# Optimization experiments

Hardware: AMD Instinct MI355X
Metric: run time of the kernel (lower is better)

The kernel has to match this reference:

```python
import jax, jax.numpy as jnp
import numpy as np

B, D, F, T, H = 256, 128, 8, 128, 128


def setup_inputs() -> dict:
    key = jax.random.key(0)
    ks = jax.random.split(key, 6)
    inp = jax.random.normal(ks[0], (B, D, F, T), jnp.float32)
    # encode_attn: Linear(F*T + 2*H -> 1); weight laid out as [hidden | cell | x]
    w_attn = jax.random.normal(ks[1], (F * T + 2 * H,), jnp.float32) * 0.02
    b_attn = jax.random.normal(ks[2], (), jnp.float32) * 0.02
    # LSTM (single layer), PyTorch gate order i, f, g, o
    W_ih = jax.random.normal(ks[3], (4 * H, D * F), jnp.float32) * 0.02
    W_hh = jax.random.normal(ks[4], (4 * H, H), jnp.float32) * 0.02
    b_ih = jax.random.normal(ks[5], (4 * H,), jnp.float32) * 0.02
    b_hh = jnp.zeros((4 * H,), jnp.float32)
    return {"input": inp, "w_attn": w_attn, "b_attn": b_attn,
            "W_ih": W_ih, "W_hh": W_hh, "b_ih": b_ih, "b_hh": b_hh}


def reference(input, w_attn, b_attn, W_ih, W_hh, b_ih, b_hh):
    Bd, Dd, Fd, Td = input.shape
    Hd = W_hh.shape[1]
    # split attention weight per cat order: (hidden_state, cell_state, x)
    w_h = w_attn[:Hd]
    w_c = w_attn[Hd:2 * Hd]
    w_x = w_attn[2 * Hd:]
    x_flat = input.reshape(Bd, Dd, Fd * Td)           # [B, D, F*T]
    ex = x_flat @ w_x                                  # [B, D], constant over t
    xs = jnp.moveaxis(input, 3, 0)                     # [T, B, D, F]

    def step(carry, x_t):
        h, c = carry                                   # [B, H] each
        # attention logits: h/c contributions are per-batch scalars broadcast over drives
        e = ex + (h @ w_h + c @ w_c + b_attn)[:, None]  # [B, D]
        a = jax.nn.softmax(e, axis=-1)                 # softmax over drives
        x_hat = (a[:, :, None] * x_t).reshape(Bd, Dd * Fd)  # [B, D*F]
        gates = x_hat @ W_ih.T + h @ W_hh.T + b_ih + b_hh   # [B, 4H]
        i, f, g, o = jnp.split(gates, 4, axis=-1)
        c_new = jax.nn.sigmoid(f) * c + jax.nn.sigmoid(i) * jnp.tanh(g)
        h_new = jax.nn.sigmoid(o) * jnp.tanh(c_new)
        return (h_new, c_new), h_new

    h0 = jnp.zeros((Bd, Hd), input.dtype)
    c0 = jnp.zeros((Bd, Hd), input.dtype)
    _, hs = jax.lax.scan(step, (h0, c0), xs)           # hs: [T, B, H]
    return jnp.transpose(hs, (1, 0, 2))                # [B, T, H] == hidden_states[:, 1:]
```

## Files before the change

### kernel.cpp

```cpp
#include <hip/hip_runtime.h>
#include <cstdint>
#include <cstddef>

#define Bn 256
#define Dn 128
#define Fn 8
#define Tn 128
#define Hn 128
#define Kn 1024
#define Mn 512
#define GXP 130

typedef float f32x4 __attribute__((ext_vector_type(4)));
typedef short s16x8 __attribute__((ext_vector_type(8)));
typedef _Float16 h16x2 __attribute__((ext_vector_type(2)));

#if defined(__has_builtin)
#if __has_builtin(__builtin_amdgcn_fdot2)
#define HAVE_FDOT2 1
#else
#define HAVE_FDOT2 0
#endif
#else
#define HAVE_FDOT2 0
#endif

__device__ __forceinline__ unsigned short f32_to_bf16_rne(float f) {
  union { float f; uint32_t u; } v; v.f = f;
  uint32_t u = v.u;
  u += 0x7fffu + ((u >> 16) & 1u);
  return (unsigned short)(u >> 16);
}
__device__ __forceinline__ float bf16_to_f32(unsigned short h) {
  union { uint32_t u; float f; } v; v.u = ((uint32_t)h) << 16;
  return v.f;
}
__device__ __forceinline__ float sigm(float x) { return 1.0f / (1.0f + __expf(-x)); }
__device__ __forceinline__ float tanh_fast(float x) { return 1.0f - 2.0f / (__expf(2.0f * x) + 1.0f); }

__global__ __launch_bounds__(256) void k_softmax_a(const float* __restrict__ input,
                                                   const float* __restrict__ w_attn,
                                                   float* __restrict__ a_out) {
  __shared__ float wx[Kn];
  __shared__ float exs[Dn];
  __shared__ float red[8];
  const int tid = threadIdx.x;
  const int b = blockIdx.x;
  ((float4*)wx)[tid] = ((const float4*)(w_attn + 2 * Hn))[tid];
  __syncthreads();
  const int w = tid >> 6, lane = tid & 63;
  const float4* wx4 = (const float4*)wx;
  for (int it = 0; it < 32; ++it) {
    const int d = it * 4 + w;
    const float4* xp = (const float4*)(input + ((size_t)b * Dn + d) * Kn);
    float acc = 0.f;
#pragma unroll
    for (int r = 0; r < 4; ++r) {
      float4 x = xp[lane + r * 64];
      float4 ww = wx4[lane + r * 64];
      acc += x.x * ww.x + x.y * ww.y + x.z * ww.z + x.w * ww.w;
    }
#pragma unroll
    for (int off = 32; off; off >>= 1) acc += __shfl_xor(acc, off);
    if (lane == 0) exs[d] = acc;
  }
  __syncthreads();
  float v = (tid < Dn) ? exs[tid] : -3.4e38f;
  float m = v;
#pragma unroll
  for (int off = 32; off; off >>= 1) m = fmaxf(m, __shfl_xor(m, off));
  if (lane == 0) red[w] = m;
  __syncthreads();
  m = fmaxf(fmaxf(red[0], red[1]), fmaxf(red[2], red[3]));
  float e = (tid < Dn) ? __expf(v - m) : 0.f;
  float s = e;
#pragma unroll
  for (int off = 32; off; off >>= 1) s += __shfl_xor(s, off);
  if (lane == 0) red[4 + w] = s;
  __syncthreads();
  s = red[4] + red[5] + red[6] + red[7];
  if (tid < Dn) a_out[b * Dn + tid] = e / s;
}

__global__ __launch_bounds__(256) void k_prep_wih(const float* __restrict__ W_ih,
                                                  unsigned short* __restrict__ whi,
                                                  unsigned short* __restrict__ wlo) {
  const int gid = blockIdx.x * 256 + threadIdx.x;
  const int lane = gid & 63;
  const int kt = (gid >> 6) & 31;
  const int mt = gid >> 11;
  const int row = mt * 16 + (lane & 15);
  const int col = kt * 32 + (lane >> 4) * 8;
  const float* src = W_ih + row * Kn + col;
  unsigned short hi8[8], lo8[8];
#pragma unroll
  for (int j = 0; j < 8; ++j) {
    float wv = src[j];
    unsigned short h = f32_to_bf16_rne(wv);
    hi8[j] = h;
    lo8[j] = f32_to_bf16_rne(wv - bf16_to_f32(h));
  }
  uint4 ph, pl;
  ph.x = (uint32_t)hi8[0] | ((uint32_t)hi8[1] << 16);
  ph.y = (uint32_t)hi8[2] | ((uint32_t)hi8[3] << 16);
  ph.z = (uint32_t)hi8[4] | ((uint32_t)hi8[5] << 16);
  ph.w = (uint32_t)hi8[6] | ((uint32_t)hi8[7] << 16);
  pl.x = (uint32_t)lo8[0] | ((uint32_t)lo8[1] << 16);
  pl.y = (uint32_t)lo8[2] | ((uint32_t)lo8[3] << 16);
  pl.z = (uint32_t)lo8[4] | ((uint32_t)lo8[5] << 16);
  pl.w = (uint32_t)lo8[6] | ((uint32_t)lo8[7] << 16);
  ((uint4*)whi)[gid] = ph;
  ((uint4*)wlo)[gid] = pl;
}

#define SM_A    133120
#define SM_G    133632
#define SM_H2   135680
#define SM_H32  135936
#define SM_TOT  136512

__global__ __launch_bounds__(512, 2) void k_fused(
    const float* __restrict__ input, const float* __restrict__ a_in,
    const unsigned short* __restrict__ whi, const unsigned short* __restrict__ wlo,
    const float* __restrict__ W_hh, const float* __restrict__ b_ih,
    const float* __restrict__ b_hh, float* __restrict__ out) {
  __shared__ __align__(16) unsigned char smem[SM_TOT];
  _Float16* gx = (_Float16*)smem;
  unsigned short* bb = (unsigned short*)smem;
  float* a_lds = (float*)(smem + SM_A);
  float* gstep = (float*)(smem + SM_G);
  _Float16* h2l = (_Float16*)(smem + SM_H2);
  float* h32 = (float*)(smem + SM_H32);

  const int tid = threadIdx.x;
  const int b = blockIdx.x;
  const int w = tid >> 6;
  const int lane = tid & 63;
  const int quad = lane >> 4;
  const int l15 = lane & 15;

  if (tid < Dn) a_lds[tid] = a_in[b * Dn + tid];

  f32x4 acc[4][8];
#pragma unroll
  for (int i = 0; i < 4; ++i)
#pragma unroll
    for (int j = 0; j < 8; ++j) {
      f32x4 z = {0.f, 0.f, 0.f, 0.f};
      acc[i][j] = z;
    }

  const int st_t = ((tid >> 6) & 1) * 64 + (tid & 63);
  const int kb2 = tid >> 7;
  const float* xb = input + (size_t)b * Kn * Tn;

  __syncthreads();

  for (int kt = 0; kt < 16; ++kt) {
    const int k0 = kt * 64;
#pragma unroll
    for (int hf = 0; hf < 2; ++hf) {
      const int kb = kb2 + hf * 4;
      const float av = a_lds[kt * 8 + kb];
      const float* col = xb + (size_t)(k0 + kb * 8) * Tn + st_t;
      unsigned short hx[8];
#pragma unroll
      for (int jj = 0; jj < 8; ++jj) hx[jj] = f32_to_bf16_rne(av * col[jj * Tn]);
      uint4 pk;
      pk.x = (uint32_t)hx[0] | ((uint32_t)hx[1] << 16);
      pk.y = (uint32_t)hx[2] | ((uint32_t)hx[3] << 16);
      pk.z = (uint32_t)hx[4] | ((uint32_t)hx[5] << 16);
      pk.w = (uint32_t)hx[6] | ((uint32_t)hx[7] << 16);
      ((uint4*)bb)[kb * 128 + st_t] = pk;
    }
    __syncthreads();
#pragma unroll
    for (int kf = 0; kf < 2; ++kf) {
      const int ktg = kt * 2 + kf;
      s16x8 afh[4], afl[4];
#pragma unroll
      for (int mt = 0; mt < 4; ++mt) {
        const int mtg = w * 4 + mt;
        const size_t fo = ((size_t)(mtg * 32 + ktg) * 64 + lane) * 8;
        afh[mt] = *(const s16x8*)(whi + fo);
        afl[mt] = *(const s16x8*)(wlo + fo);
      }
      s16x8 bfr[8];
#pragma unroll
      for (int nt = 0; nt < 8; ++nt) {
        const int chunk = (kf * 4 + quad) * 128 + nt * 16 + l15;
        bfr[nt] = *(const s16x8*)(bb + chunk * 8);
      }
#pragma unroll
      for (int mt = 0; mt < 4; ++mt)
#pragma unroll
        for (int nt = 0; nt < 8; ++nt) {
          acc[mt][nt] = __builtin_amdgcn_mfma_f32_16x16x32_bf16(afh[mt], bfr[nt], acc[mt][nt], 0, 0, 0);
          acc[mt][nt] = __builtin_amdgcn_mfma_f32_16x16x32_bf16(afl[mt], bfr[nt], acc[mt][nt], 0, 0, 0);
        }
    }
    __syncthreads();
  }

#pragma unroll
  for (int mt = 0; mt < 4; ++mt)
#pragma unroll
    for (int nt = 0; nt < 8; ++nt)
#pragma unroll
      for (int r = 0; r < 4; ++r) {
        const int j = w * 64 + mt * 16 + quad * 4 + r;
        const int t = nt * 16 + l15;
        gx[j * GXP + t] = (_Float16)acc[mt][nt][r];
      }

  const int j = tid;
  const float bsum = b_ih[j] + b_hh[j];
#if HAVE_FDOT2
  h16x2 wreg[64];
  {
    const float2* wrow = (const float2*)(W_hh + (size_t)j * Hn);
#pragma unroll
    for (int kk = 0; kk < 64; ++kk) {
      float2 w2 = wrow[kk];
      h16x2 t2;
      t2.x = (_Float16)w2.x;
      t2.y = (_Float16)w2.y;
      wreg[kk] = t2;
    }
  }
#else
  float wreg[128];
  {
    const float4* wrow = (const float4*)(W_hh + (size_t)j * Hn);
#pragma unroll
    for (int kk = 0; kk < 32; ++kk) {
      float4 w4 = wrow[kk];
      wreg[kk * 4 + 0] = w4.x;
      wreg[kk * 4 + 1] = w4.y;
      wreg[kk * 4 + 2] = w4.z;
      wreg[kk * 4 + 3] = w4.w;
    }
  }
#endif
  if (tid < Dn) {
    h2l[tid] = (_Float16)0.f;
    h32[tid] = 0.f;
  }
  float c_st = 0.f;
  __syncthreads();

  float* outp = out + (size_t)b * Tn * Hn;
  for (int t = 0; t < Tn; ++t) {
    float a0 = bsum + (float)gx[j * GXP + t];
    float a1 = 0.f, a2 = 0.f, a3 = 0.f;
#if HAVE_FDOT2
    const h16x2* hc = (const h16x2*)h2l;
#pragma unroll
    for (int kk = 0; kk < 16; ++kk) {
      a0 = __builtin_amdgcn_fdot2(wreg[kk * 4 + 0], hc[kk * 4 + 0], a0, false);
      a1 = __builtin_amdgcn_fdot2(wreg[kk * 4 + 1], hc[kk * 4 + 1], a1, false);
      a2 = __builtin_amdgcn_fdot2(wreg[kk * 4 + 2], hc[kk * 4 + 2], a2, false);
      a3 = __builtin_amdgcn_fdot2(wreg[kk * 4 + 3], hc[kk * 4 + 3], a3, false);
    }
#else
    const float4* hc4 = (const float4*)h32;
#pragma unroll
    for (int kk = 0; kk < 32; ++kk) {
      float4 h4 = hc4[kk];
      a0 = fmaf(wreg[kk * 4 + 0], h4.x, a0);
      a1 = fmaf(wreg[kk * 4 + 1], h4.y, a1);
      a2 = fmaf(wreg[kk * 4 + 2], h4.z, a2);
      a3 = fmaf(wreg[kk * 4 + 3], h4.w, a3);
    }
#endif
    gstep[j] = a0 + a1 + a2 + a3;
    __syncthreads();
    if (tid < Hn) {
      const int d = tid;
      const float gi = gstep[d];
      const float gf = gstep[Hn + d];
      const float gg = gstep[2 * Hn + d];
      const float go = gstep[3 * Hn + d];
      c_st = sigm(gf) * c_st + sigm(gi) * tanh_fast(gg);
      const float hnew = sigm(go) * tanh_fast(c_st);
      outp[t * Hn + d] = hnew;
      h2l[d] = (_Float16)hnew;
      h32[d] = hnew;
    }
    __syncthreads();
  }
}

extern "C" void kernel_launch(void* const* d_in, const int* in_sizes, int n_in,
                              void* d_out, int out_size, void* d_ws, size_t ws_size,
                              hipStream_t stream) {
  (void)in_sizes; (void)n_in; (void)out_size; (void)ws_size;
  const float* input = (const float*)d_in[0];
  const float* w_attn = (const float*)d_in[1];
  const float* W_ih = (const float*)d_in[3];
  const float* W_hh = (const float*)d_in[4];
  const float* b_ih = (const float*)d_in[5];
  const float* b_hh = (const float*)d_in[6];
  float* out = (float*)d_out;

  float* a_ws = (float*)d_ws;
  unsigned short* whi = (unsigned short*)((char*)d_ws + 131072);
  unsigned short* wlo = (unsigned short*)((char*)d_ws + 131072 + 1048576);

  k_softmax_a<<<Bn, 256, 0, stream>>>(input, w_attn, a_ws);
  k_prep_wih<<<256, 256, 0, stream>>>(W_ih, whi, wlo);
  k_fused<<<Bn, 512, 0, stream>>>(input, a_ws, whi, wlo, W_hh, b_ih, b_hh, out);
}
```

Measured before the change: 398.9 us.

## Split fused kernel into parallel gate GEMM and separate recurrence kernel

Splits the single per-batch fused kernel (input-projection GEMM plus LSTM recurrence) into a gate kernel launched with four blocks per batch that each own a quarter of the gate rows, and a separate recurrence kernel that reads the fp16 gate projections through global memory. The gate kernel double-buffers the LDS tile so the next k-slice is loaded while the current one feeds the MFMAs, and it XOR-swizzles LDS addresses to reduce bank conflicts. The attention-logit dot products now run one wave per (batch, drive) row across many more blocks, with the softmax moved into the gate kernel. W_hh is pre-packed to fp16 in a transposed layout for coalesced loads. The cost is an extra global round trip for the gate projections and more kernel launches, in exchange for more parallelism in the GEMM phase.

```diff
diff --git a/kernel.cpp b/kernel.cpp
--- a/kernel.cpp
+++ b/kernel.cpp
@@ -9,7 +9,6 @@
 #define Hn 128
 #define Kn 1024
 #define Mn 512
-#define GXP 130
 
 typedef float f32x4 __attribute__((ext_vector_type(4)));
 typedef short s16x8 __attribute__((ext_vector_type(8)));
@@ -31,55 +30,30 @@
   u += 0x7fffu + ((u >> 16) & 1u);
   return (unsigned short)(u >> 16);
 }
-__device__ __forceinline__ float bf16_to_f32(unsigned short h) {
-  union { uint32_t u; float f; } v; v.u = ((uint32_t)h) << 16;
-  return v.f;
-}
 __device__ __forceinline__ float sigm(float x) { return 1.0f / (1.0f + __expf(-x)); }
 __device__ __forceinline__ float tanh_fast(float x) { return 1.0f - 2.0f / (__expf(2.0f * x) + 1.0f); }
 
-__global__ __launch_bounds__(256) void k_softmax_a(const float* __restrict__ input,
-                                                   const float* __restrict__ w_attn,
-                                                   float* __restrict__ a_out) {
+__global__ __launch_bounds__(256) void k_ex(const float* __restrict__ input,
+                                            const float* __restrict__ w_attn,
+                                            float* __restrict__ ex) {
   __shared__ float wx[Kn];
-  __shared__ float exs[Dn];
-  __shared__ float red[8];
   const int tid = threadIdx.x;
-  const int b = blockIdx.x;
   ((float4*)wx)[tid] = ((const float4*)(w_attn + 2 * Hn))[tid];
   __syncthreads();
   const int w = tid >> 6, lane = tid & 63;
+  const int gid = blockIdx.x * 4 + w;
+  const float4* xp = (const float4*)(input + (size_t)gid * Kn);
   const float4* wx4 = (const float4*)wx;
-  for (int it = 0; it < 32; ++it) {
-    const int d = it * 4 + w;
-    const float4* xp = (const float4*)(input + ((size_t)b * Dn + d) * Kn);
-    float acc = 0.f;
-#pragma unroll
-    for (int r = 0; r < 4; ++r) {
-      float4 x = xp[lane + r * 64];
-      float4 ww = wx4[lane + r * 64];
-      acc += x.x * ww.x + x.y * ww.y + x.z * ww.z + x.w * ww.w;
-    }
-#pragma unroll
-    for (int off = 32; off; off >>= 1) acc += __shfl_xor(acc, off);
-    if (lane == 0) exs[d] = acc;
-  }
-  __syncthreads();
-  float v = (tid < Dn) ? exs[tid] : -3.4e38f;
-  float m = v;
-#pragma unroll
-  for (int off = 32; off; off >>= 1) m = fmaxf(m, __shfl_xor(m, off));
-  if (lane == 0) red[w] = m;
-  __syncthreads();
-  m = fmaxf(fmaxf(red[0], red[1]), fmaxf(red[2], red[3]));
-  float e = (tid < Dn) ? __expf(v - m) : 0.f;
-  float s = e;
-#pragma unroll
-  for (int off = 32; off; off >>= 1) s += __shfl_xor(s, off);
-  if (lane == 0) red[4 + w] = s;
-  __syncthreads();
-  s = red[4] + red[5] + red[6] + red[7];
-  if (tid < Dn) a_out[b * Dn + tid] = e / s;
+  float acc = 0.f;
+#pragma unroll
+  for (int r = 0; r < 4; ++r) {
+    float4 x = xp[lane + r * 64];
+    float4 ww = wx4[lane + r * 64];
+    acc += x.x * ww.x + x.y * ww.y + x.z * ww.z + x.w * ww.w;
+  }
+#pragma unroll
+  for (int off = 32; off; off >>= 1) acc += __shfl_xor(acc, off);
+  if (lane == 0) ex[gid] = acc;
 }
 
 __global__ __launch_bounds__(256) void k_prep_wih(const float* __restrict__ W_ih,
@@ -98,7 +72,8 @@
     float wv = src[j];
     unsigned short h = f32_to_bf16_rne(wv);
     hi8[j] = h;
-    lo8[j] = f32_to_bf16_rne(wv - bf16_to_f32(h));
+    union { uint32_t u; float f; } hb; hb.u = ((uint32_t)h) << 16;
+    lo8[j] = f32_to_bf16_rne(wv - hb.f);
   }
   uint4 ph, pl;
   ph.x = (uint32_t)hi8[0] | ((uint32_t)hi8[1] << 16);
@@ -113,146 +88,212 @@
   ((uint4*)wlo)[gid] = pl;
 }
 
-#define SM_A    133120
-#define SM_G    133632
-#define SM_H2   135680
-#define SM_H32  135936
-#define SM_TOT  136512
-
-__global__ __launch_bounds__(512, 2) void k_fused(
-    const float* __restrict__ input, const float* __restrict__ a_in,
+__global__ __launch_bounds__(256) void k_prep_whh(const float* __restrict__ W_hh,
+                                                  uint32_t* __restrict__ whhp) {
+  const int g = blockIdx.x * 256 + threadIdx.x;
+  const int j = g & 511, kk = g >> 9;
+  float2 wv = ((const float2*)(W_hh + (size_t)j * Hn))[kk];
+  h16x2 t2; t2.x = (_Float16)wv.x; t2.y = (_Float16)wv.y;
+  union { h16x2 h; uint32_t u; } cv; cv.h = t2;
+  whhp[kk * 512 + j] = cv.u;
+}
+
+__global__ __launch_bounds__(256, 3) void k_gates(
+    const float* __restrict__ input, const float* __restrict__ ex,
     const unsigned short* __restrict__ whi, const unsigned short* __restrict__ wlo,
-    const float* __restrict__ W_hh, const float* __restrict__ b_ih,
-    const float* __restrict__ b_hh, float* __restrict__ out) {
-  __shared__ __align__(16) unsigned char smem[SM_TOT];
-  _Float16* gx = (_Float16*)smem;
-  unsigned short* bb = (unsigned short*)smem;
-  float* a_lds = (float*)(smem + SM_A);
-  float* gstep = (float*)(smem + SM_G);
-  _Float16* h2l = (_Float16*)(smem + SM_H2);
-  float* h32 = (float*)(smem + SM_H32);
+    unsigned short* __restrict__ gx) {
+  __shared__ __align__(16) unsigned char smem[34816];
+  __shared__ float a_lds[Dn];
+  __shared__ float sred[8];
+  unsigned short* buf0 = (unsigned short*)smem;
+  unsigned short* buf1 = buf0 + 8192;
+  _Float16* lds_out = (_Float16*)smem;
 
   const int tid = threadIdx.x;
-  const int b = blockIdx.x;
+  const int b = blockIdx.x >> 2;
+  const int p = blockIdx.x & 3;
   const int w = tid >> 6;
   const int lane = tid & 63;
   const int quad = lane >> 4;
   const int l15 = lane & 15;
 
-  if (tid < Dn) a_lds[tid] = a_in[b * Dn + tid];
-
-  f32x4 acc[4][8];
-#pragma unroll
-  for (int i = 0; i < 4; ++i)
-#pragma unroll
-    for (int j = 0; j < 8; ++j) {
-      f32x4 z = {0.f, 0.f, 0.f, 0.f};
-      acc[i][j] = z;
-    }
-
-  const int st_t = ((tid >> 6) & 1) * 64 + (tid & 63);
-  const int kb2 = tid >> 7;
+  float v = (tid < Dn) ? ex[b * Dn + tid] : -3.4e38f;
+  float m = v;
+#pragma unroll
+  for (int off = 32; off; off >>= 1) m = fmaxf(m, __shfl_xor(m, off));
+  if (lane == 0) sred[w] = m;
+  __syncthreads();
+  m = fmaxf(fmaxf(sred[0], sred[1]), fmaxf(sred[2], sred[3]));
+  float e = (tid < Dn) ? __expf(v - m) : 0.f;
+  float s = e;
+#pragma unroll
+  for (int off = 32; off; off >>= 1) s += __shfl_xor(s, off);
+  if (lane == 0) sred[4 + w] = s;
+  __syncthreads();
+  s = sred[4] + sred[5] + sred[6] + sred[7];
+  if (tid < Dn) a_lds[tid] = e / s;
+
+  f32x4 acc[2][8];
+#pragma unroll
+  for (int i = 0; i < 2; ++i)
+#pragma unroll
+    for (int j = 0; j < 8; ++j) { f32x4 z = {0.f, 0.f, 0.f, 0.f}; acc[i][j] = z; }
+
+  const int kb = tid >> 5;
+  const int t0 = (tid & 31) * 4;
   const float* xb = input + (size_t)b * Kn * Tn;
 
   __syncthreads();
 
-  for (int kt = 0; kt < 16; ++kt) {
-    const int k0 = kt * 64;
-#pragma unroll
-    for (int hf = 0; hf < 2; ++hf) {
-      const int kb = kb2 + hf * 4;
-      const float av = a_lds[kt * 8 + kb];
-      const float* col = xb + (size_t)(k0 + kb * 8) * Tn + st_t;
+  {
+    float4 xr[8];
+    const float* src = xb + (size_t)(kb * 8) * Tn + t0;
+#pragma unroll
+    for (int j = 0; j < 8; ++j) xr[j] = *(const float4*)(src + (size_t)j * Tn);
+    const float av = a_lds[kb];
+#pragma unroll
+    for (int i = 0; i < 4; ++i) {
       unsigned short hx[8];
 #pragma unroll
-      for (int jj = 0; jj < 8; ++jj) hx[jj] = f32_to_bf16_rne(av * col[jj * Tn]);
+      for (int j = 0; j < 8; ++j) hx[j] = f32_to_bf16_rne(av * ((const float*)&xr[j])[i]);
       uint4 pk;
       pk.x = (uint32_t)hx[0] | ((uint32_t)hx[1] << 16);
       pk.y = (uint32_t)hx[2] | ((uint32_t)hx[3] << 16);
       pk.z = (uint32_t)hx[4] | ((uint32_t)hx[5] << 16);
       pk.w = (uint32_t)hx[6] | ((uint32_t)hx[7] << 16);
-      ((uint4*)bb)[kb * 128 + st_t] = pk;
-    }
-    __syncthreads();
+      const int tsw = (t0 + i) ^ ((kb & 1) << 2);
+      *(uint4*)(buf0 + (size_t)(kb * 128 + tsw) * 8) = pk;
+    }
+  }
+  __syncthreads();
+
+  for (int kt = 0; kt < 16; ++kt) {
+    unsigned short* cur = (kt & 1) ? buf1 : buf0;
+    unsigned short* nxt = (kt & 1) ? buf0 : buf1;
+    float4 xr[8];
+    if (kt < 15) {
+      const float* src = xb + (size_t)((kt + 1) * 64 + kb * 8) * Tn + t0;
+#pragma unroll
+      for (int j = 0; j < 8; ++j) xr[j] = *(const float4*)(src + (size_t)j * Tn);
+    }
 #pragma unroll
     for (int kf = 0; kf < 2; ++kf) {
       const int ktg = kt * 2 + kf;
-      s16x8 afh[4], afl[4];
-#pragma unroll
-      for (int mt = 0; mt < 4; ++mt) {
-        const int mtg = w * 4 + mt;
+      s16x8 afh[2], afl[2];
+#pragma unroll
+      for (int mt = 0; mt < 2; ++mt) {
+        const int mtg = p * 8 + w * 2 + mt;
         const size_t fo = ((size_t)(mtg * 32 + ktg) * 64 + lane) * 8;
         afh[mt] = *(const s16x8*)(whi + fo);
         afl[mt] = *(const s16x8*)(wlo + fo);
       }
       s16x8 bfr[8];
+      const int kbr = kf * 4 + quad;
 #pragma unroll
       for (int nt = 0; nt < 8; ++nt) {
-        const int chunk = (kf * 4 + quad) * 128 + nt * 16 + l15;
-        bfr[nt] = *(const s16x8*)(bb + chunk * 8);
-      }
-#pragma unroll
-      for (int mt = 0; mt < 4; ++mt)
+        const int tsw = (nt * 16 + l15) ^ ((kbr & 1) << 2);
+        bfr[nt] = *(const s16x8*)(cur + (size_t)(kbr * 128 + tsw) * 8);
+      }
+#pragma unroll
+      for (int mt = 0; mt < 2; ++mt)
 #pragma unroll
         for (int nt = 0; nt < 8; ++nt) {
           acc[mt][nt] = __builtin_amdgcn_mfma_f32_16x16x32_bf16(afh[mt], bfr[nt], acc[mt][nt], 0, 0, 0);
           acc[mt][nt] = __builtin_amdgcn_mfma_f32_16x16x32_bf16(afl[mt], bfr[nt], acc[mt][nt], 0, 0, 0);
         }
     }
+    if (kt < 15) {
+      const float av = a_lds[(kt + 1) * 8 + kb];
+#pragma unroll
+      for (int i = 0; i < 4; ++i) {
+        unsigned short hx[8];
+#pragma unroll
+        for (int j = 0; j < 8; ++j) hx[j] = f32_to_bf16_rne(av * ((const float*)&xr[j])[i]);
+        uint4 pk;
+        pk.x = (uint32_t)hx[0] | ((uint32_t)hx[1] << 16);
+        pk.y = (uint32_t)hx[2] | ((uint32_t)hx[3] << 16);
+        pk.z = (uint32_t)hx[4] | ((uint32_t)hx[5] << 16);
+        pk.w = (uint32_t)hx[6] | ((uint32_t)hx[7] << 16);
+        const int tsw = (t0 + i) ^ ((kb & 1) << 2);
+        *(uint4*)(nxt + (size_t)(kb * 128 + tsw) * 8) = pk;
+      }
+    }
     __syncthreads();
   }
 
 #pragma unroll
-  for (int mt = 0; mt < 4; ++mt)
+  for (int mt = 0; mt < 2; ++mt)
 #pragma unroll
     for (int nt = 0; nt < 8; ++nt)
 #pragma unroll
       for (int r = 0; r < 4; ++r) {
-        const int j = w * 64 + mt * 16 + quad * 4 + r;
-        const int t = nt * 16 + l15;
-        gx[j * GXP + t] = (_Float16)acc[mt][nt][r];
-      }
-
+        const int jl = (w * 2 + mt) * 16 + quad * 4 + r;
+        lds_out[jl * 136 + nt * 16 + l15] = (_Float16)acc[mt][nt][r];
+      }
+  __syncthreads();
+  {
+    const int jr = tid >> 1, half = tid & 1;
+    const uint4* lsrc = (const uint4*)(lds_out + jr * 136 + half * 64);
+    uint4* gdst = (uint4*)(gx + ((size_t)(b * Mn + p * 128 + jr)) * Tn + half * 64);
+#pragma unroll
+    for (int i = 0; i < 8; ++i) gdst[i] = lsrc[i];
+  }
+}
+
+__global__ __launch_bounds__(512) void k_rec(
+    const unsigned short* __restrict__ gx, const uint32_t* __restrict__ whhp,
+    const float* __restrict__ b_ih, const float* __restrict__ b_hh,
+    float* __restrict__ out) {
+  __shared__ __align__(16) unsigned short gxl[512 * 132];
+  __shared__ float gstep[Mn];
+  __shared__ __align__(4) _Float16 h2l[Hn];
+  __shared__ float h32[Hn];
+
+  const int tid = threadIdx.x;
+  const int b = blockIdx.x;
+
+  {
+    const int seg = tid & 3, rr = tid >> 2;
+#pragma unroll
+    for (int it = 0; it < 4; ++it) {
+      const int row = it * 128 + rr;
+      const uint4* gsrc = (const uint4*)(gx + ((size_t)b * Mn + row) * Tn + seg * 32);
+      uint2* dst = (uint2*)(gxl + row * 132 + seg * 32);
+#pragma unroll
+      for (int q = 0; q < 4; ++q) {
+        uint4 v = gsrc[q];
+        uint2 a0 = {v.x, v.y}, a1 = {v.z, v.w};
+        dst[q * 2] = a0;
+        dst[q * 2 + 1] = a1;
+      }
+    }
+  }
   const int j = tid;
   const float bsum = b_ih[j] + b_hh[j];
 #if HAVE_FDOT2
   h16x2 wreg[64];
-  {
-    const float2* wrow = (const float2*)(W_hh + (size_t)j * Hn);
-#pragma unroll
-    for (int kk = 0; kk < 64; ++kk) {
-      float2 w2 = wrow[kk];
-      h16x2 t2;
-      t2.x = (_Float16)w2.x;
-      t2.y = (_Float16)w2.y;
-      wreg[kk] = t2;
-    }
+#pragma unroll
+  for (int kk = 0; kk < 64; ++kk) {
+    union { uint32_t u; h16x2 h; } cv; cv.u = whhp[kk * 512 + j];
+    wreg[kk] = cv.h;
   }
 #else
   float wreg[128];
-  {
-    const float4* wrow = (const float4*)(W_hh + (size_t)j * Hn);
-#pragma unroll
-    for (int kk = 0; kk < 32; ++kk) {
-      float4 w4 = wrow[kk];
-      wreg[kk * 4 + 0] = w4.x;
-      wreg[kk * 4 + 1] = w4.y;
-      wreg[kk * 4 + 2] = w4.z;
-      wreg[kk * 4 + 3] = w4.w;
-    }
+#pragma unroll
+  for (int kk = 0; kk < 64; ++kk) {
+    union { uint32_t u; h16x2 h; } cv; cv.u = whhp[kk * 512 + j];
+    wreg[kk * 2] = (float)cv.h.x;
+    wreg[kk * 2 + 1] = (float)cv.h.y;
   }
 #endif
-  if (tid < Dn) {
-    h2l[tid] = (_Float16)0.f;
-    h32[tid] = 0.f;
-  }
+  if (tid < Hn) { h2l[tid] = (_Float16)0.f; h32[tid] = 0.f; }
   float c_st = 0.f;
   __syncthreads();
 
   float* outp = out + (size_t)b * Tn * Hn;
   for (int t = 0; t < Tn; ++t) {
-    float a0 = bsum + (float)gx[j * GXP + t];
-    float a1 = 0.f, a2 = 0.f, a3 = 0.f;
+    const _Float16 gxv = *(const _Float16*)&gxl[j * 132 + t];
+    float a0 = 0.f, a1 = 0.f, a2 = 0.f, a3 = 0.f;
 #if HAVE_FDOT2
     const h16x2* hc = (const h16x2*)h2l;
 #pragma unroll
@@ -263,26 +304,24 @@
       a3 = __builtin_amdgcn_fdot2(wreg[kk * 4 + 3], hc[kk * 4 + 3], a3, false);
     }
 #else
-    const float4* hc4 = (const float4*)h32;
 #pragma unroll
     for (int kk = 0; kk < 32; ++kk) {
-      float4 h4 = hc4[kk];
-      a0 = fmaf(wreg[kk * 4 + 0], h4.x, a0);
-      a1 = fmaf(wreg[kk * 4 + 1], h4.y, a1);
-      a2 = fmaf(wreg[kk * 4 + 2], h4.z, a2);
-      a3 = fmaf(wreg[kk * 4 + 3], h4.w, a3);
+      a0 = fmaf(wreg[kk * 4 + 0], h32[kk * 4 + 0], a0);
+      a1 = fmaf(wreg[kk * 4 + 1], h32[kk * 4 + 1], a1);
+      a2 = fmaf(wreg[kk * 4 + 2], h32[kk * 4 + 2], a2);
+      a3 = fmaf(wreg[kk * 4 + 3], h32[kk * 4 + 3], a3);
     }
 #endif
-    gstep[j] = a0 + a1 + a2 + a3;
+    gstep[j] = (a0 + a1) + (a2 + a3) + bsum + (float)gxv;
     __syncthreads();
+    const int d = tid & 127;
+    const float gi = gstep[d];
+    const float gf = gstep[Hn + d];
+    const float gg = gstep[2 * Hn + d];
+    const float go = gstep[3 * Hn + d];
+    c_st = sigm(gf) * c_st + sigm(gi) * tanh_fast(gg);
+    const float hnew = sigm(go) * tanh_fast(c_st);
     if (tid < Hn) {
-      const int d = tid;
-      const float gi = gstep[d];
-      const float gf = gstep[Hn + d];
-      const float gg = gstep[2 * Hn + d];
-      const float go = gstep[3 * Hn + d];
-      c_st = sigm(gf) * c_st + sigm(gi) * tanh_fast(gg);
-      const float hnew = sigm(go) * tanh_fast(c_st);
       outp[t * Hn + d] = hnew;
       h2l[d] = (_Float16)hnew;
       h32[d] = hnew;
@@ -303,11 +342,16 @@
   const float* b_hh = (const float*)d_in[6];
   float* out = (float*)d_out;
 
-  float* a_ws = (float*)d_ws;
-  unsigned short* whi = (unsigned short*)((char*)d_ws + 131072);
-  unsigned short* wlo = (unsigned short*)((char*)d_ws + 131072 + 1048576);
-
-  k_softmax_a<<<Bn, 256, 0, stream>>>(input, w_attn, a_ws);
+  char* ws = (char*)d_ws;
+  float* ex = (float*)ws;
+  unsigned short* whi = (unsigned short*)(ws + 131072);
+  unsigned short* wlo = (unsigned short*)(ws + 1179648);
+  uint32_t* whhp = (uint32_t*)(ws + 2228224);
+  unsigned short* gxw = (unsigned short*)(ws + 2359296);
+
+  k_ex<<<8192, 256, 0, stream>>>(input, w_attn, ex);
   k_prep_wih<<<256, 256, 0, stream>>>(W_ih, whi, wlo);
-  k_fused<<<Bn, 512, 0, stream>>>(input, a_ws, whi, wlo, W_hh, b_ih, b_hh, out);
-}
+  k_prep_whh<<<128, 256, 0, stream>>>(W_hh, whhp);
+  k_gates<<<1024, 256, 0, stream>>>(input, ex, whi, wlo, gxw);
+  k_rec<<<Bn, 512, 0, stream>>>(gxw, whhp, b_ih, b_hh, out);
+}
```

After: 434.6 us. 9.0% more time.
